# Performance work log

Hardware: AMD Instinct MI355X
Metric: run time of the kernel (lower is better)

The kernel has to match this reference:

```python
import jax, jax.numpy as jnp
import numpy as np

N = 100000
F = 512
D = 128
E = 1600000

def setup_inputs() -> dict:
    key = jax.random.key(0)
    k1, k2, k3, k4, k5 = jax.random.split(key, 5)
    feature = jax.random.normal(k1, (N, F), dtype=jnp.float32)
    W = jax.random.normal(k2, (F, D), dtype=jnp.float32) * (1.0 / np.sqrt(D))
    bias = jax.random.normal(k3, (D,), dtype=jnp.float32) * (1.0 / np.sqrt(D))
    edge_vals = jax.random.uniform(k4, (E,), dtype=jnp.float32)
    edge_index = jax.random.randint(k5, (2, E), 0, N, dtype=jnp.int32)
    return {"feature": feature, "W": W, "bias": bias,
            "edge_vals": edge_vals, "edge_index": edge_index}

def reference(feature, W, bias, edge_vals, edge_index):
    # support = relu(feature @ W)                          [N, D]
    support = jax.nn.relu(feature @ W)
    row, col = edge_index[0], edge_index[1]
    # spmm(adj, support): gather source rows, scale, scatter-add to dest rows
    msgs = edge_vals[:, None] * support[col]               # [E, D]
    agg = jax.ops.segment_sum(msgs, row, num_segments=feature.shape[0])
    # adj_low = adj + I  ->  identity contributes +support; then + bias
    return agg + support + bias
```

## Files before the change

### kernel.cpp

```cpp
#include <hip/hip_runtime.h>
#include <hip/hip_bf16.h>

typedef __attribute__((ext_vector_type(8))) __bf16 bf16x8;
typedef __attribute__((ext_vector_type(4))) float f32x4;

#define F_DIM 512
#define D_DIM 128
#define RPB 128
#define MAXBUK 1024
#define BIN_CHUNK 8192

__device__ __forceinline__ unsigned short f32_to_bf16_rn(float x) {
    union { float f; unsigned u; } v; v.f = x;
    unsigned u = v.u;
    unsigned rounded = u + 0x7fffu + ((u >> 16) & 1u);
    return (unsigned short)(rounded >> 16);
}
__device__ __forceinline__ float bf16_to_f32(unsigned short u) {
    return __uint_as_float((unsigned)u << 16);
}

__global__ void wt_kernel(const float* __restrict__ W, unsigned short* __restrict__ Wt) {
    int idx = blockIdx.x * blockDim.x + threadIdx.x;
    int n = idx >> 9;
    int k = idx & 511;
    Wt[idx] = f32_to_bf16_rn(W[k * D_DIM + n]);
}

__global__ __launch_bounds__(256) void gemm_relu_pipe(
    const float* __restrict__ A,
    const unsigned short* __restrict__ Bt,
    unsigned short* __restrict__ Sb,
    int Nrows)
{
    __shared__ unsigned short Al[2 * 128 * 40];
    __shared__ unsigned short Bl[2 * 128 * 40];

    const int tid  = threadIdx.x;
    const int wave = tid >> 6;
    const int lane = tid & 63;
    const int g    = lane >> 4;
    const int r16  = lane & 15;
    const int m0   = blockIdx.x * 128;

    const int srow = tid >> 1;
    const int kh   = tid & 1;
    int arow = m0 + srow;
    if (arow >= Nrows) arow = Nrows - 1;
    const float*          aptr = A  + (size_t)arow * F_DIM + kh * 16;
    const unsigned short* bptr = Bt + (size_t)srow * F_DIM + kh * 16;
    const int woff = srow * 40 + kh * 16;

    float4 ar0, ar1, ar2, ar3;
    uint4  br0, br1;

    auto loadAB = [&](int ks) {
        const float4* pa = (const float4*)(aptr + ks * 32);
        ar0 = pa[0]; ar1 = pa[1]; ar2 = pa[2]; ar3 = pa[3];
        const uint4* pb = (const uint4*)(bptr + ks * 32);
        br0 = pb[0]; br1 = pb[1];
    };
    auto storeAB = [&](int buf) {
        union { uint4 q[2]; __bf16 h[16]; } u;
        u.h[0]=(__bf16)ar0.x;  u.h[1]=(__bf16)ar0.y;  u.h[2]=(__bf16)ar0.z;  u.h[3]=(__bf16)ar0.w;
        u.h[4]=(__bf16)ar1.x;  u.h[5]=(__bf16)ar1.y;  u.h[6]=(__bf16)ar1.z;  u.h[7]=(__bf16)ar1.w;
        u.h[8]=(__bf16)ar2.x;  u.h[9]=(__bf16)ar2.y;  u.h[10]=(__bf16)ar2.z; u.h[11]=(__bf16)ar2.w;
        u.h[12]=(__bf16)ar3.x; u.h[13]=(__bf16)ar3.y; u.h[14]=(__bf16)ar3.z; u.h[15]=(__bf16)ar3.w;
        unsigned short* aw = Al + buf * 5120 + woff;
        unsigned short* bw = Bl + buf * 5120 + woff;
        *(uint4*)aw       = u.q[0];
        *(uint4*)(aw + 8) = u.q[1];
        *(uint4*)bw       = br0;
        *(uint4*)(bw + 8) = br1;
    };

    f32x4 acc[2][8];
#pragma unroll
    for (int i = 0; i < 2; ++i)
#pragma unroll
        for (int j = 0; j < 8; ++j) acc[i][j] = (f32x4)0.0f;

    loadAB(0);
    storeAB(0);
    __syncthreads();

#pragma unroll
    for (int ks = 0; ks < 16; ++ks) {
        const int cur = ks & 1;
        if (ks < 15) loadAB(ks + 1);

        const unsigned short* Ab = Al + cur * 5120;
        const unsigned short* Bb = Bl + cur * 5120;
        bf16x8 af0 = *(const bf16x8*)&Ab[(wave * 32 +      r16) * 40 + g * 8];
        bf16x8 af1 = *(const bf16x8*)&Ab[(wave * 32 + 16 + r16) * 40 + g * 8];
#pragma unroll
        for (int nf = 0; nf < 8; ++nf) {
            bf16x8 bf = *(const bf16x8*)&Bb[(nf * 16 + r16) * 40 + g * 8];
            acc[0][nf] = __builtin_amdgcn_mfma_f32_16x16x32_bf16(af0, bf, acc[0][nf], 0, 0, 0);
            acc[1][nf] = __builtin_amdgcn_mfma_f32_16x16x32_bf16(af1, bf, acc[1][nf], 0, 0, 0);
        }

        if (ks < 15) storeAB(cur ^ 1);
        __syncthreads();
    }

#pragma unroll
    for (int mf = 0; mf < 2; ++mf) {
#pragma unroll
        for (int nf = 0; nf < 8; ++nf) {
#pragma unroll
            for (int r = 0; r < 4; ++r) {
                int row = m0 + wave * 32 + mf * 16 + g * 4 + r;
                if (row < Nrows) {
                    float v = acc[mf][nf][r];
                    Sb[(size_t)row * D_DIM + nf * 16 + r16] = f32_to_bf16_rn(v > 0.f ? v : 0.f);
                }
            }
        }
    }
}

__global__ void cursor_init_kernel(int* __restrict__ cursor, int nbuk, int cap) {
    int i = blockIdx.x * blockDim.x + threadIdx.x;
    if (i < nbuk) cursor[i] = i * cap;
}

__global__ __launch_bounds__(256) void bin_kernel(
    const int* __restrict__ ei, const float* __restrict__ ev,
    int* __restrict__ cursor, uint2* __restrict__ ecv, int E, int nbuk)
{
    __shared__ int cnt[MAXBUK];
    __shared__ int bas[MAXBUK];
    const int tid = threadIdx.x;
    const int e0 = blockIdx.x * BIN_CHUNK;
    const int e1 = min(e0 + BIN_CHUNK, E);

    for (int i = tid; i < nbuk; i += 256) cnt[i] = 0;
    __syncthreads();
    for (int e = e0 + tid; e < e1; e += 256)
        atomicAdd(&cnt[ei[e] >> 7], 1);
    __syncthreads();
    for (int i = tid; i < nbuk; i += 256) {
        int c = cnt[i];
        bas[i] = c ? atomicAdd(&cursor[i], c) : 0;
        cnt[i] = 0;
    }
    __syncthreads();
    for (int e = e0 + tid; e < e1; e += 256) {
        int r = ei[e];
        int b = r >> 7;
        int slot = atomicAdd(&cnt[b], 1);
        uint2 cv;
        cv.x = ((unsigned)ei[E + e] << 7) | (unsigned)(r & 127);
        cv.y = __float_as_uint(ev[e]);
        ecv[(size_t)bas[b] + slot] = cv;
    }
}

__global__ __launch_bounds__(256) void bsort_kernel(
    const uint2* __restrict__ ecv, const int* __restrict__ cursor,
    uint2* __restrict__ ecv2, int* __restrict__ rowoff, int* __restrict__ rowcnt,
    int cap, int Nrows)
{
    __shared__ int cnt[RPB];
    __shared__ int base[RPB];
    const int tid = threadIdx.x;
    const int b   = blockIdx.x;
    const int beg = b * cap;
    const int end = cursor[b];

    if (tid < RPB) cnt[tid] = 0;
    __syncthreads();
    for (int i = beg + tid; i < end; i += 256)
        atomicAdd(&cnt[ecv[i].x & 127], 1);
    __syncthreads();
    if (tid < 64) {
        int carry = 0;
#pragma unroll
        for (int c = 0; c < 2; ++c) {
            int idx = c * 64 + tid;
            int v = cnt[idx];
            int orig = v;
            for (int d = 1; d < 64; d <<= 1) {
                int t = __shfl_up(v, d, 64);
                if (tid >= d) v += t;
            }
            base[idx] = carry + v - orig;
            carry += __shfl(v, 63, 64);
        }
    }
    __syncthreads();
    if (tid < RPB) {
        int r = b * RPB + tid;
        if (r < Nrows) {
            rowoff[r] = beg + base[tid];
            rowcnt[r] = cnt[tid];
        }
        cnt[tid] = 0;
    }
    __syncthreads();
    for (int i = beg + tid; i < end; i += 256) {
        uint2 cv = ecv[i];
        int rl = cv.x & 127;
        int slot = atomicAdd(&cnt[rl], 1);
        ecv2[(size_t)beg + base[rl] + slot] = cv;
    }
}

__global__ __launch_bounds__(256) void accum_kernel(
    const uint2* __restrict__ ecv2, const int* __restrict__ rowoff,
    const int* __restrict__ rowcnt, const unsigned short* __restrict__ Sb,
    const float* __restrict__ bias, float* __restrict__ out, int n)
{
    int wid = (blockIdx.x * 256 + threadIdx.x) >> 6;
    if (wid >= n) return;
    int lane = threadIdx.x & 63;
    int c2 = lane * 2;

    int start = rowoff[wid];
    int end   = start + rowcnt[wid];

    float ax = 0.f, ay = 0.f;
    int i = start;
    for (; i + 3 < end; i += 4) {
        uint2 cv0 = ecv2[i];
        uint2 cv1 = ecv2[i + 1];
        uint2 cv2 = ecv2[i + 2];
        uint2 cv3 = ecv2[i + 3];
        ushort2 s0 = *(const ushort2*)&Sb[(size_t)(cv0.x >> 7) * D_DIM + c2];
        ushort2 s1 = *(const ushort2*)&Sb[(size_t)(cv1.x >> 7) * D_DIM + c2];
        ushort2 s2 = *(const ushort2*)&Sb[(size_t)(cv2.x >> 7) * D_DIM + c2];
        ushort2 s3 = *(const ushort2*)&Sb[(size_t)(cv3.x >> 7) * D_DIM + c2];
        float v0 = __uint_as_float(cv0.y);
        float v1 = __uint_as_float(cv1.y);
        float v2 = __uint_as_float(cv2.y);
        float v3 = __uint_as_float(cv3.y);
        ax += v0 * bf16_to_f32(s0.x) + v1 * bf16_to_f32(s1.x)
            + v2 * bf16_to_f32(s2.x) + v3 * bf16_to_f32(s3.x);
        ay += v0 * bf16_to_f32(s0.y) + v1 * bf16_to_f32(s1.y)
            + v2 * bf16_to_f32(s2.y) + v3 * bf16_to_f32(s3.y);
    }
    for (; i < end; ++i) {
        uint2 cv = ecv2[i];
        ushort2 s = *(const ushort2*)&Sb[(size_t)(cv.x >> 7) * D_DIM + c2];
        float v = __uint_as_float(cv.y);
        ax += v * bf16_to_f32(s.x);
        ay += v * bf16_to_f32(s.y);
    }

    ushort2 so = *(const ushort2*)&Sb[(size_t)wid * D_DIM + c2];
    float2 b = *(const float2*)&bias[c2];
    float2 o;
    o.x = ax + bf16_to_f32(so.x) + b.x;
    o.y = ay + bf16_to_f32(so.y) + b.y;
    *(float2*)&out[(size_t)wid * D_DIM + c2] = o;
}

extern "C" void kernel_launch(void* const* d_in, const int* in_sizes, int n_in,
                              void* d_out, int out_size, void* d_ws, size_t ws_size,
                              hipStream_t stream) {
    const float* feature = (const float*)d_in[0];
    const float* W       = (const float*)d_in[1];
    const float* bias    = (const float*)d_in[2];
    const float* ev      = (const float*)d_in[3];
    const int*   ei      = (const int*)d_in[4];
    float* out = (float*)d_out;

    const int N = in_sizes[0] / F_DIM;
    const int E = in_sizes[3];
    const int nbuk = (N + RPB - 1) / RPB;
    int cap = (E + nbuk - 1) / nbuk;
    cap = cap + cap / 4 + 256;

    char* ws = (char*)d_ws;
    size_t cur = 0;
    auto alloc = [&](size_t bytes) -> void* {
        void* p = ws + cur;
        cur = (cur + bytes + 255) & ~(size_t)255;
        return p;
    };
    unsigned short* Sb     = (unsigned short*)alloc((size_t)N * D_DIM * 2);
    unsigned short* Wt     = (unsigned short*)alloc((size_t)D_DIM * F_DIM * 2);
    int*            cursor = (int*)alloc((size_t)nbuk * 4);
    int*            rowoff = (int*)alloc((size_t)N * 4);
    int*            rowcnt = (int*)alloc((size_t)N * 4);
    uint2*          ecv    = (uint2*)alloc(((size_t)nbuk * cap + BIN_CHUNK) * 8);
    uint2*          ecv2   = (uint2*)alloc(((size_t)nbuk * cap + BIN_CHUNK) * 8);
    (void)ws_size;

    wt_kernel<<<(F_DIM * D_DIM) / 256, 256, 0, stream>>>(W, Wt);
    gemm_relu_pipe<<<(N + 127) / 128, 256, 0, stream>>>(feature, Wt, Sb, N);
    cursor_init_kernel<<<(nbuk + 255) / 256, 256, 0, stream>>>(cursor, nbuk, cap);
    bin_kernel<<<(E + BIN_CHUNK - 1) / BIN_CHUNK, 256, 0, stream>>>(ei, ev, cursor, ecv, E, nbuk);
    bsort_kernel<<<nbuk, 256, 0, stream>>>(ecv, cursor, ecv2, rowoff, rowcnt, cap, N);
    accum_kernel<<<(N + 3) / 4, 256, 0, stream>>>(ecv2, rowoff, rowcnt, Sb, bias, out, N);
}
```

Before: 222.0 us.

## Stream fp32 A tiles into LDS via global_load_lds and fuse prep kernels

The GEMM now loads fp32 feature tiles straight into swizzled LDS with global_load_lds instead of staging them through registers as bf16. The tile is converted to bf16 at fragment-read time, and B fragments are read directly from global memory (which should hit L2) instead of LDS. The W transpose and cursor init are merged into one prep kernel to save a launch, and BIN_CHUNK is halved to give the binning kernel more blocks. The cost is twice the LDS footprint per stage and extra conversion work in the inner loop.

```diff
diff --git a/kernel.cpp b/kernel.cpp
--- a/kernel.cpp
+++ b/kernel.cpp
@@ -8,7 +8,7 @@
 #define D_DIM 128
 #define RPB 128
 #define MAXBUK 1024
-#define BIN_CHUNK 8192
+#define BIN_CHUNK 4096
 
 __device__ __forceinline__ unsigned short f32_to_bf16_rn(float x) {
     union { float f; unsigned u; } v; v.f = x;
@@ -20,21 +20,39 @@
     return __uint_as_float((unsigned)u << 16);
 }
 
-__global__ void wt_kernel(const float* __restrict__ W, unsigned short* __restrict__ Wt) {
-    int idx = blockIdx.x * blockDim.x + threadIdx.x;
-    int n = idx >> 9;
-    int k = idx & 511;
-    Wt[idx] = f32_to_bf16_rn(W[k * D_DIM + n]);
-}
-
-__global__ __launch_bounds__(256) void gemm_relu_pipe(
+__device__ __forceinline__ void gload_lds16(const void* g, void* l) {
+    __builtin_amdgcn_global_load_lds(
+        (const __attribute__((address_space(1))) void*)g,
+        (__attribute__((address_space(3))) void*)l, 16, 0, 0);
+}
+
+__device__ __forceinline__ bf16x8 cvt8(float4 a, float4 b) {
+    bf16x8 r;
+    r[0] = (__bf16)a.x; r[1] = (__bf16)a.y; r[2] = (__bf16)a.z; r[3] = (__bf16)a.w;
+    r[4] = (__bf16)b.x; r[5] = (__bf16)b.y; r[6] = (__bf16)b.z; r[7] = (__bf16)b.w;
+    return r;
+}
+
+__global__ void prep_kernel(const float* __restrict__ W, unsigned short* __restrict__ Wt,
+                            int* __restrict__ cursor, int nbuk, int cap) {
+    int b = blockIdx.x;
+    if (b < 256) {
+        int idx = b * 256 + threadIdx.x;
+        int n = idx >> 9;
+        int k = idx & 511;
+        Wt[idx] = f32_to_bf16_rn(W[k * D_DIM + n]);
+    } else {
+        for (int i = threadIdx.x; i < nbuk; i += 256) cursor[i] = i * cap;
+    }
+}
+
+__global__ __launch_bounds__(256) void gemm_relu_gll(
     const float* __restrict__ A,
     const unsigned short* __restrict__ Bt,
     unsigned short* __restrict__ Sb,
     int Nrows)
 {
-    __shared__ unsigned short Al[2 * 128 * 40];
-    __shared__ unsigned short Bl[2 * 128 * 40];
+    __shared__ float Al[2 * 128 * 32];
 
     const int tid  = threadIdx.x;
     const int wave = tid >> 6;
@@ -43,36 +61,18 @@
     const int r16  = lane & 15;
     const int m0   = blockIdx.x * 128;
 
-    const int srow = tid >> 1;
-    const int kh   = tid & 1;
-    int arow = m0 + srow;
-    if (arow >= Nrows) arow = Nrows - 1;
-    const float*          aptr = A  + (size_t)arow * F_DIM + kh * 16;
-    const unsigned short* bptr = Bt + (size_t)srow * F_DIM + kh * 16;
-    const int woff = srow * 40 + kh * 16;
-
-    float4 ar0, ar1, ar2, ar3;
-    uint4  br0, br1;
-
-    auto loadAB = [&](int ks) {
-        const float4* pa = (const float4*)(aptr + ks * 32);
-        ar0 = pa[0]; ar1 = pa[1]; ar2 = pa[2]; ar3 = pa[3];
-        const uint4* pb = (const uint4*)(bptr + ks * 32);
-        br0 = pb[0]; br1 = pb[1];
-    };
-    auto storeAB = [&](int buf) {
-        union { uint4 q[2]; __bf16 h[16]; } u;
-        u.h[0]=(__bf16)ar0.x;  u.h[1]=(__bf16)ar0.y;  u.h[2]=(__bf16)ar0.z;  u.h[3]=(__bf16)ar0.w;
-        u.h[4]=(__bf16)ar1.x;  u.h[5]=(__bf16)ar1.y;  u.h[6]=(__bf16)ar1.z;  u.h[7]=(__bf16)ar1.w;
-        u.h[8]=(__bf16)ar2.x;  u.h[9]=(__bf16)ar2.y;  u.h[10]=(__bf16)ar2.z; u.h[11]=(__bf16)ar2.w;
-        u.h[12]=(__bf16)ar3.x; u.h[13]=(__bf16)ar3.y; u.h[14]=(__bf16)ar3.z; u.h[15]=(__bf16)ar3.w;
-        unsigned short* aw = Al + buf * 5120 + woff;
-        unsigned short* bw = Bl + buf * 5120 + woff;
-        *(uint4*)aw       = u.q[0];
-        *(uint4*)(aw + 8) = u.q[1];
-        *(uint4*)bw       = br0;
-        *(uint4*)(bw + 8) = br1;
-    };
+    const float* gsrc[4];
+    int ldsoff[4];
+#pragma unroll
+    for (int it = 0; it < 4; ++it) {
+        int i    = it * 256 + tid;
+        int row  = i >> 3;
+        int csrc = (i & 7) ^ (row & 7);
+        int arow = m0 + row;
+        if (arow >= Nrows) arow = Nrows - 1;
+        gsrc[it]   = A + (size_t)arow * F_DIM + csrc * 4;
+        ldsoff[it] = (it * 256 + wave * 64) * 16;
+    }
 
     f32x4 acc[2][8];
 #pragma unroll
@@ -80,27 +80,42 @@
 #pragma unroll
         for (int j = 0; j < 8; ++j) acc[i][j] = (f32x4)0.0f;
 
-    loadAB(0);
-    storeAB(0);
+#pragma unroll
+    for (int it = 0; it < 4; ++it)
+        gload_lds16(gsrc[it], (char*)Al + ldsoff[it]);
     __syncthreads();
 
 #pragma unroll
     for (int ks = 0; ks < 16; ++ks) {
         const int cur = ks & 1;
-        if (ks < 15) loadAB(ks + 1);
-
-        const unsigned short* Ab = Al + cur * 5120;
-        const unsigned short* Bb = Bl + cur * 5120;
-        bf16x8 af0 = *(const bf16x8*)&Ab[(wave * 32 +      r16) * 40 + g * 8];
-        bf16x8 af1 = *(const bf16x8*)&Ab[(wave * 32 + 16 + r16) * 40 + g * 8];
+        if (ks < 15) {
+#pragma unroll
+            for (int it = 0; it < 4; ++it)
+                gload_lds16(gsrc[it] + (ks + 1) * 32,
+                            (char*)Al + (cur ^ 1) * 16384 + ldsoff[it]);
+        }
+
+        bf16x8 bfr[8];
+#pragma unroll
+        for (int nf = 0; nf < 8; ++nf)
+            bfr[nf] = *(const bf16x8*)&Bt[(size_t)(nf * 16 + r16) * F_DIM + ks * 32 + g * 8];
+
+        const char* Ab = (const char*)Al + cur * 16384;
+        bf16x8 af[2];
+#pragma unroll
+        for (int mf = 0; mf < 2; ++mf) {
+            int row = wave * 32 + mf * 16 + r16;
+            int sw  = row & 7;
+            float4 lo = *(const float4*)(Ab + row * 128 + ((2 * g)     ^ sw) * 16);
+            float4 hi = *(const float4*)(Ab + row * 128 + ((2 * g + 1) ^ sw) * 16);
+            af[mf] = cvt8(lo, hi);
+        }
+
 #pragma unroll
         for (int nf = 0; nf < 8; ++nf) {
-            bf16x8 bf = *(const bf16x8*)&Bb[(nf * 16 + r16) * 40 + g * 8];
-            acc[0][nf] = __builtin_amdgcn_mfma_f32_16x16x32_bf16(af0, bf, acc[0][nf], 0, 0, 0);
-            acc[1][nf] = __builtin_amdgcn_mfma_f32_16x16x32_bf16(af1, bf, acc[1][nf], 0, 0, 0);
-        }
-
-        if (ks < 15) storeAB(cur ^ 1);
+            acc[0][nf] = __builtin_amdgcn_mfma_f32_16x16x32_bf16(af[0], bfr[nf], acc[0][nf], 0, 0, 0);
+            acc[1][nf] = __builtin_amdgcn_mfma_f32_16x16x32_bf16(af[1], bfr[nf], acc[1][nf], 0, 0, 0);
+        }
         __syncthreads();
     }
 
@@ -118,11 +133,6 @@
             }
         }
     }
-}
-
-__global__ void cursor_init_kernel(int* __restrict__ cursor, int nbuk, int cap) {
-    int i = blockIdx.x * blockDim.x + threadIdx.x;
-    if (i < nbuk) cursor[i] = i * cap;
 }
 
 __global__ __launch_bounds__(256) void bin_kernel(
@@ -288,9 +298,8 @@
     uint2*          ecv2   = (uint2*)alloc(((size_t)nbuk * cap + BIN_CHUNK) * 8);
     (void)ws_size;
 
-    wt_kernel<<<(F_DIM * D_DIM) / 256, 256, 0, stream>>>(W, Wt);
-    gemm_relu_pipe<<<(N + 127) / 128, 256, 0, stream>>>(feature, Wt, Sb, N);
-    cursor_init_kernel<<<(nbuk + 255) / 256, 256, 0, stream>>>(cursor, nbuk, cap);
+    prep_kernel<<<257, 256, 0, stream>>>(W, Wt, cursor, nbuk, cap);
+    gemm_relu_gll<<<(N + 127) / 128, 256, 0, stream>>>(feature, Wt, Sb, N);
     bin_kernel<<<(E + BIN_CHUNK - 1) / BIN_CHUNK, 256, 0, stream>>>(ei, ev, cursor, ecv, E, nbuk);
     bsort_kernel<<<nbuk, 256, 0, stream>>>(ecv, cursor, ecv2, rowoff, rowcnt, cap, N);
     accum_kernel<<<(N + 3) / 4, 256, 0, stream>>>(ecv2, rowoff, rowcnt, Sb, bias, out, N);
```

Result: slower. 250.1 us (+12.7%).
